# Optimization experiments

Hardware: AMD Instinct MI355X
Metric: run time of the kernel (lower is better)

The kernel has to match this reference:

```python
import jax, jax.numpy as jnp
import numpy as np
from functools import partial

B, T, C, HS = 8, 2048, 2048, 64
H = C // HS
LAYER_ID, N_LAYER, DIVISOR = 12, 24, 8.0


def setup_inputs() -> dict:
    key = jax.random.key(0)
    ks = jax.random.split(key, 6)
    x = jax.random.normal(ks[0], (B, T, C), jnp.float32)
    # faithful RWKV5 parameter initialization
    r01 = LAYER_ID / (N_LAYER - 1)
    r10 = 1.0 - LAYER_ID / N_LAYER
    ddd = np.arange(C, dtype=np.float64) / C
    tmk = (ddd ** r10).reshape(1, 1, C)
    tmv = tmk + 0.3 * r01
    tmr = (ddd ** (0.5 * r10)).reshape(1, 1, C)
    tmg = tmr.copy()
    n = np.arange(C, dtype=np.float64)
    decay = -6.0 + 5.0 * (n / (C - 1)) ** (0.7 + 1.3 * r01)
    zig = ((n + 1) % 3 - 1) * 0.1
    faaaa = r01 * (1.0 - n / (C - 1)) + zig
    f32 = lambda a: jnp.asarray(a, jnp.float32)
    W = lambda k: jax.random.normal(k, (C, C), jnp.float32) * 0.02
    return {
        'x': x,
        'time_mix_k': f32(tmk), 'time_mix_v': f32(tmv),
        'time_mix_r': f32(tmr), 'time_mix_g': f32(tmg),
        'time_decay': f32(decay.reshape(H, HS)),
        'time_faaaa': f32(faaaa.reshape(H, HS)),
        'Wr': W(ks[1]), 'Wk': W(ks[2]), 'Wv': W(ks[3]),
        'Wg': W(ks[4]), 'Wo': W(ks[5]),
        'ln_w': jnp.ones((C,), jnp.float32),
        'ln_b': jnp.zeros((C,), jnp.float32),
    }


def _wkv5(r, k, v, w, u):
    # r,k,v: [B,T,H,N]; w,u: [H,N]; sequential decayed linear attention
    rT = jnp.swapaxes(r, 0, 1)  # [T,B,H,N]
    kT = jnp.swapaxes(k, 0, 1)
    vT = jnp.swapaxes(v, 0, 1)
    wI = w[None, :, :, None]  # decay on key dim i of state S[b,h,i,j]
    uI = u[None, :, :, None]

    def step(S, rkv):
        r_t, k_t, v_t = rkv
        kv = jnp.einsum('bhi,bhj->bhij', k_t, v_t)
        y = jnp.einsum('bhi,bhij->bhj', r_t, S + uI * kv)
        return wI * S + kv, y

    S0 = jnp.zeros((r.shape[0], r.shape[2], r.shape[3], r.shape[3]), r.dtype)
    _, ys = jax.lax.scan(step, S0, (rT, kT, vT))
    return jnp.swapaxes(ys, 0, 1)  # [B,T,H,N]


def reference(x, time_mix_k, time_mix_v, time_mix_r, time_mix_g,
              time_decay, time_faaaa, Wr, Wk, Wv, Wg, Wo, ln_w, ln_b):
    # time shift: prepend zero row, drop last (ZeroPad2d((0,0,1,-1)))
    xx = jnp.pad(x, ((0, 0), (1, 0), (0, 0)))[:, :-1]
    xk = x * time_mix_k + xx * (1.0 - time_mix_k)
    xv = x * time_mix_v + xx * (1.0 - time_mix_v)
    xr = x * time_mix_r + xx * (1.0 - time_mix_r)
    xg = x * time_mix_g + xx * (1.0 - time_mix_g)
    r = (xr @ Wr).reshape(B, T, H, HS)
    k = (xk @ Wk).reshape(B, T, H, HS)
    v = (xv @ Wv).reshape(B, T, H, HS)
    g = jax.nn.silu(xg @ Wg)
    w = jnp.exp(-jnp.exp(time_decay))  # [H,N]
    y = _wkv5(r, k, v, w, time_faaaa)  # [B,T,H,N]
    # GroupNorm(H groups) over head_size, after /head_size_divisor
    yh = y / DIVISOR
    mu = jnp.mean(yh, axis=-1, keepdims=True)
    var = jnp.var(yh, axis=-1, keepdims=True)
    yn = (yh - mu) * jax.lax.rsqrt(var + 1e-5)
    yn = yn * ln_w.reshape(H, HS) + ln_b.reshape(H, HS)
    out = (yn.reshape(B, T, C) * g) @ Wo
    return out
```

## Files before the change

### kernel.cpp

```cpp
#include <hip/hip_runtime.h>
#include <hip/hip_bf16.h>

typedef __bf16 bf16_t;
typedef __bf16 bf16x8 __attribute__((ext_vector_type(8)));
typedef float f32x4 __attribute__((ext_vector_type(4)));

#define Bn 8
#define Tn 2048
#define Cn 2048
#define Hn 32
#define HSn 64
#define CT 64

static const long SZ = (long)Bn * Tn * Cn;

__device__ __forceinline__ void g2l16(const void* g, void* l) {
  __builtin_amdgcn_global_load_lds((const __attribute__((address_space(1))) void*)g,
                                   (__attribute__((address_space(3))) void*)l,
                                   16, 0, 0);
}

template <int CTRL>
__device__ __forceinline__ float dppadd(float x) {
  int yi = __builtin_amdgcn_update_dpp(__float_as_int(x), __float_as_int(x),
                                       CTRL, 0xf, 0xf, false);
  return x + __int_as_float(yi);
}

__global__ __launch_bounds__(256)
void transps(const float* w0, const float* w1, const float* w2,
             const float* w3, const float* w4, bf16_t* oh, bf16_t* ol)
{
  const float* Ws[5] = {w0, w1, w2, w3, w4};
  const float* W = Ws[blockIdx.z];
  const long base = (long)blockIdx.z * ((long)Cn * Cn);
  __shared__ float tile[64][65];
  const int xx = threadIdx.x & 63;
  const int y4 = threadIdx.x >> 6;
  const int bx = blockIdx.x * 64, by = blockIdx.y * 64;
#pragma unroll
  for (int i = 0; i < 16; ++i) {
    int row = i * 4 + y4;
    tile[row][xx] = W[(long)(by + row) * Cn + bx + xx];
  }
  __syncthreads();
#pragma unroll
  for (int i = 0; i < 16; ++i) {
    int row = i * 4 + y4;
    float v = tile[xx][row];
    bf16_t hi = (bf16_t)v;
    long o = base + (long)(bx + row) * Cn + by + xx;
    oh[o] = hi;
    ol[o] = (bf16_t)(v - (float)hi);
  }
}

template <int AMODE, int EMODE>
__global__ __launch_bounds__(512)
void gemmx(const float* __restrict__ X, const float* __restrict__ tm,
           const bf16_t* __restrict__ Ah, const bf16_t* __restrict__ Al,
           const bf16_t* __restrict__ BTh, const bf16_t* __restrict__ BTl,
           void* __restrict__ Cp,
           const bf16_t* __restrict__ Zh, const bf16_t* __restrict__ Zl,
           bf16_t* __restrict__ Gh, bf16_t* __restrict__ Gl)
{
  __shared__ __align__(16) bf16_t lAh[2][256 * 32];
  __shared__ __align__(16) bf16_t lAl[2][256 * 32];
  __shared__ __align__(16) bf16_t lBh[2][256 * 32];
  __shared__ __align__(16) bf16_t lBl[2][256 * 32];

  const int tid = threadIdx.x;
  const int wv = tid >> 6;
  const int lane = tid & 63;
  const int wmw = (wv >> 2) & 1;
  const int wnw = wv & 3;
  const long m0 = (long)blockIdx.y * 256;
  const int n0 = blockIdx.x * 256;

  const int e0 = tid * 8;
  const int e1 = 4096 + tid * 8;
  const int r0 = tid >> 2;
  const int s0 = tid & 3;
  const int c0 = (s0 ^ ((r0 >> 1) & 3)) << 3;
  const long aoff0 = (m0 + r0) * Cn + c0;
  const long aoff1 = (m0 + r0 + 128) * Cn + c0;
  const long boff0 = (long)(n0 + r0) * Cn + c0;
  const long boff1 = (long)(n0 + r0 + 128) * Cn + c0;
  const bool p0ok = ((int)(m0 & (Tn - 1)) | r0) != 0;

  const int kg = lane >> 4;
  const int lr = lane & 15;
  const int kS = (kg ^ ((lr >> 1) & 3)) * 8;

  auto mixA = [&](long kc2, int dst) {
    float xf[16], pf[16], tf[8];
    const long a0 = aoff0 + kc2, a1 = aoff1 + kc2;
    *(f32x4*)&xf[0]  = *(const f32x4*)&X[a0];
    *(f32x4*)&xf[4]  = *(const f32x4*)&X[a0 + 4];
    *(f32x4*)&xf[8]  = *(const f32x4*)&X[a1];
    *(f32x4*)&xf[12] = *(const f32x4*)&X[a1 + 4];
    if (p0ok) {
      *(f32x4*)&pf[0] = *(const f32x4*)&X[a0 - Cn];
      *(f32x4*)&pf[4] = *(const f32x4*)&X[a0 - Cn + 4];
    } else {
#pragma unroll
      for (int q = 0; q < 8; ++q) pf[q] = 0.f;
    }
    *(f32x4*)&pf[8]  = *(const f32x4*)&X[a1 - Cn];
    *(f32x4*)&pf[12] = *(const f32x4*)&X[a1 - Cn + 4];
    *(f32x4*)&tf[0] = *(const f32x4*)&tm[kc2 + c0];
    *(f32x4*)&tf[4] = *(const f32x4*)&tm[kc2 + c0 + 4];
    bf16x8 h0, l0, h1, l1;
#pragma unroll
    for (int q = 0; q < 8; ++q) {
      float o0 = pf[q] + tf[q] * (xf[q] - pf[q]);
      bf16_t hi0 = (bf16_t)o0;
      h0[q] = hi0; l0[q] = (bf16_t)(o0 - (float)hi0);
      float o1 = pf[8 + q] + tf[q] * (xf[8 + q] - pf[8 + q]);
      bf16_t hi1 = (bf16_t)o1;
      h1[q] = hi1; l1[q] = (bf16_t)(o1 - (float)hi1);
    }
    *(bf16x8*)&lAh[dst][e0] = h0; *(bf16x8*)&lAl[dst][e0] = l0;
    *(bf16x8*)&lAh[dst][e1] = h1; *(bf16x8*)&lAl[dst][e1] = l1;
  };

  if constexpr (AMODE == 0) {
    mixA(0, 0);
    g2l16(BTh + boff0, &lBh[0][e0]);
    g2l16(BTh + boff1, &lBh[0][e1]);
    __builtin_amdgcn_sched_barrier(0);
    g2l16(BTl + boff0, &lBl[0][e0]);
    g2l16(BTl + boff1, &lBl[0][e1]);
  } else {
    g2l16(Ah + aoff0, &lAh[0][e0]);
    g2l16(Ah + aoff1, &lAh[0][e1]);
    g2l16(BTh + boff0, &lBh[0][e0]);
    g2l16(BTh + boff1, &lBh[0][e1]);
    __builtin_amdgcn_sched_barrier(0);
    g2l16(Al + aoff0, &lAl[0][e0]);
    g2l16(Al + aoff1, &lAl[0][e1]);
    g2l16(BTl + boff0, &lBl[0][e0]);
    g2l16(BTl + boff1, &lBl[0][e1]);
  }

  const int NT = Cn / 32;
  f32x4 acc[8][4] = {};
  bf16x8 ah[8], bh[4];

  for (int t = 0; t < NT; ++t) {
    const int cb = t & 1, nb = cb ^ 1;
    const int tn = (t + 1 < NT) ? t + 1 : 0;
    const long kc = (long)tn * 32;

    if constexpr (AMODE == 0) {
      asm volatile("s_waitcnt vmcnt(2) lgkmcnt(0)" ::: "memory");
    } else {
      asm volatile("s_waitcnt vmcnt(4)" ::: "memory");
    }
    __builtin_amdgcn_sched_barrier(0);
    __builtin_amdgcn_s_barrier();
    __builtin_amdgcn_sched_barrier(0);
    if constexpr (AMODE == 0) {
      g2l16(BTh + boff0 + kc, &lBh[nb][e0]);
      g2l16(BTh + boff1 + kc, &lBh[nb][e1]);
      g2l16(BTl + boff0 + kc, &lBl[nb][e0]);
      g2l16(BTl + boff1 + kc, &lBl[nb][e1]);
    } else {
      g2l16(Ah + aoff0 + kc, &lAh[nb][e0]);
      g2l16(Ah + aoff1 + kc, &lAh[nb][e1]);
      g2l16(BTh + boff0 + kc, &lBh[nb][e0]);
      g2l16(BTh + boff1 + kc, &lBh[nb][e1]);
    }
#pragma unroll
    for (int i = 0; i < 8; ++i)
      ah[i] = *(const bf16x8*)&lAh[cb][(wmw * 128 + i * 16 + lr) * 32 + kS];
#pragma unroll
    for (int j = 0; j < 4; ++j)
      bh[j] = *(const bf16x8*)&lBh[cb][(wnw * 64 + j * 16 + lr) * 32 + kS];
    __builtin_amdgcn_s_setprio(1);
#pragma unroll
    for (int i = 0; i < 8; ++i)
#pragma unroll
      for (int j = 0; j < 4; ++j)
        acc[i][j] = __builtin_amdgcn_mfma_f32_16x16x32_bf16(ah[i], bh[j], acc[i][j], 0, 0, 0);
    __builtin_amdgcn_s_setprio(0);
    if constexpr (AMODE == 0) mixA(kc, nb);

    asm volatile("s_waitcnt vmcnt(4)" ::: "memory");
    __builtin_amdgcn_sched_barrier(0);
    __builtin_amdgcn_s_barrier();
    __builtin_amdgcn_sched_barrier(0);
    if constexpr (AMODE == 1) {
      g2l16(Al + aoff0 + kc, &lAl[nb][e0]);
      g2l16(Al + aoff1 + kc, &lAl[nb][e1]);
      g2l16(BTl + boff0 + kc, &lBl[nb][e0]);
      g2l16(BTl + boff1 + kc, &lBl[nb][e1]);
    }
    bf16x8 al[8], bl[4];
#pragma unroll
    for (int i = 0; i < 8; ++i)
      al[i] = *(const bf16x8*)&lAl[cb][(wmw * 128 + i * 16 + lr) * 32 + kS];
#pragma unroll
    for (int j = 0; j < 4; ++j)
      bl[j] = *(const bf16x8*)&lBl[cb][(wnw * 64 + j * 16 + lr) * 32 + kS];
    __builtin_amdgcn_s_setprio(1);
#pragma unroll
    for (int i = 0; i < 8; ++i) {
#pragma unroll
      for (int j = 0; j < 4; ++j)
        acc[i][j] = __builtin_amdgcn_mfma_f32_16x16x32_bf16(al[i], bh[j], acc[i][j], 0, 0, 0);
#pragma unroll
      for (int j = 0; j < 4; ++j)
        acc[i][j] = __builtin_amdgcn_mfma_f32_16x16x32_bf16(ah[i], bl[j], acc[i][j], 0, 0, 0);
    }
    __builtin_amdgcn_s_setprio(0);
  }

  const int qr = lane >> 4;
  const int cnn = lane & 15;
#pragma unroll
  for (int i = 0; i < 8; ++i) {
#pragma unroll
    for (int j = 0; j < 4; ++j) {
#pragma unroll
      for (int rg = 0; rg < 4; ++rg) {
        long row = m0 + wmw * 128 + i * 16 + qr * 4 + rg;
        int col = n0 + wnw * 64 + j * 16 + cnn;
        long off = row * Cn + col;
        float vv = acc[i][j][rg];
        if constexpr (EMODE == 0) {
          ((bf16_t*)Cp)[off] = (bf16_t)vv;
        } else if constexpr (EMODE == 1) {
          float z = (float)Zh[off] + (float)Zl[off];
          float zg = vv / (1.f + __expf(-vv)) * z;
          bf16_t hi = (bf16_t)zg;
          Gh[off] = hi;
          Gl[off] = (bf16_t)(zg - (float)hi);
        } else if constexpr (EMODE == 2) {
          ((float*)Cp)[off] = vv;
        } else {
          bf16_t hi = (bf16_t)vv;
          Gh[off] = hi;
          Gl[off] = (bf16_t)(vv - (float)hi);
        }
      }
    }
  }
}

__global__ __launch_bounds__(512)
void wkv5(const bf16_t* Rh, const bf16_t* __restrict__ Rl,
          const bf16_t* Km, const bf16_t* __restrict__ Vm,
          const float* __restrict__ decay, const float* __restrict__ faaaa,
          const float* __restrict__ lw, const float* __restrict__ lb,
          bf16_t* Zh, bf16_t* Zl)
{
  const int bh = blockIdx.x;
  const int b = bh >> 5;
  const int h = bh & 31;
  const int tid = threadIdx.x;
  const int j = tid >> 3;
  const int ic = tid & 7;
  const int i0 = ic * 8;

  float w[8], u[8], S[8];
#pragma unroll
  for (int q = 0; q < 8; ++q) {
    w[q] = expf(-expf(decay[h * 64 + i0 + q]));
    u[q] = faaaa[h * 64 + i0 + q];
    S[q] = 0.f;
  }

  __shared__ __align__(16) float sR[2][CT * 64];
  __shared__ __align__(16) float sK[2][CT * 64];
  __shared__ __align__(16) float sV[2][CT * 64];
  __shared__ __align__(16) float sY[CT * 64];
  __shared__ float sA[2][CT];

  const int e = tid * 8;
  const int tl = e >> 6;
  const int cc = e & 63;
  const long gbase = (long)b * Tn * Cn + h * 64 + cc;

  const int wv = tid >> 6;
  const int ln = tid & 63;
  const float lwv = lw[h * 64 + ln];
  const float lbv = lb[h * 64 + ln];

  bf16x8 prh, prl, pk, pv;
  auto issue = [&](int cch) {
    const long g = gbase + (long)(cch * CT + tl) * Cn;
    prh = *(const bf16x8*)&Rh[g];
    prl = *(const bf16x8*)&Rl[g];
    pk  = *(const bf16x8*)&Km[g];
    pv  = *(const bf16x8*)&Vm[g];
  };
  auto commit = [&](int bufA) {
    float apv = 0.f;
#pragma unroll
    for (int q = 0; q < 8; ++q) {
      float rf = (float)prh[q] + (float)prl[q];
      float kf = (float)pk[q];
      sR[bufA][e + q] = rf;
      sK[bufA][e + q] = kf;
      sV[bufA][e + q] = (float)pv[q];
      apv += (rf * u[q]) * kf;
    }
    apv = dppadd<0xB1>(apv);
    apv = dppadd<0x4E>(apv);
    apv = dppadd<0x141>(apv);
    if (ic == 0) sA[bufA][tl] = apv;
  };

  issue(0); commit(0);
  __syncthreads();
  issue(1);

  const int NC = Tn / CT;
  for (int cch = 0; cch < NC; ++cch) {
    const int buf = cch & 1;
#pragma unroll 4
    for (int t = 0; t < CT; ++t) {
      float rr[8], kk[8];
      *(f32x4*)&rr[0] = *(const f32x4*)&sR[buf][t * 64 + i0];
      *(f32x4*)&rr[4] = *(const f32x4*)&sR[buf][t * 64 + i0 + 4];
      *(f32x4*)&kk[0] = *(const f32x4*)&sK[buf][t * 64 + i0];
      *(f32x4*)&kk[4] = *(const f32x4*)&sK[buf][t * 64 + i0 + 4];
      float vj = sV[buf][t * 64 + j];
      float yp = 0.f;
#pragma unroll
      for (int q = 0; q < 8; ++q) {
        yp += rr[q] * S[q];
        S[q] = w[q] * S[q] + kk[q] * vj;
      }
      yp = dppadd<0xB1>(yp);
      yp = dppadd<0x4E>(yp);
      yp = dppadd<0x141>(yp);
      if (ic == 0) sY[t * 64 + j] = (yp + sA[buf][t] * vj) * 0.125f;
    }
    if (cch + 1 < NC) commit((cch + 1) & 1);
    __syncthreads();
    if (cch + 2 < NC) issue(cch + 2);

    const long zrow0 = ((long)b * Tn + (long)cch * CT) * Cn + h * 64 + ln;
#pragma unroll
    for (int q = 0; q < 8; ++q) {
      const int t = wv * 8 + q;
      float val = sY[t * 64 + ln];
      float s = val, s2 = val * val;
      s = dppadd<0xB1>(s);   s2 = dppadd<0xB1>(s2);
      s = dppadd<0x4E>(s);   s2 = dppadd<0x4E>(s2);
      s = dppadd<0x141>(s);  s2 = dppadd<0x141>(s2);
      s = dppadd<0x140>(s);  s2 = dppadd<0x140>(s2);
      s  += __shfl_xor(s, 16);  s2 += __shfl_xor(s2, 16);
      s  += __shfl_xor(s, 32);  s2 += __shfl_xor(s2, 32);
      float mu = s * (1.f / 64.f);
      float var = fmaxf(s2 * (1.f / 64.f) - mu * mu, 0.f);
      float rs = rsqrtf(var + 1e-5f);
      float zv = (val - mu) * rs * lwv + lbv;
      bf16_t zh = (bf16_t)zv;
      Zh[zrow0 + (long)t * Cn] = zh;
      Zl[zrow0 + (long)t * Cn] = (bf16_t)(zv - (float)zh);
    }
    __syncthreads();
  }
}

extern "C" void kernel_launch(void* const* d_in, const int* in_sizes, int n_in,
                              void* d_out, int out_size, void* d_ws, size_t ws_size,
                              hipStream_t stream)
{
  const float* x    = (const float*)d_in[0];
  const float* tmk  = (const float*)d_in[1];
  const float* tmv  = (const float*)d_in[2];
  const float* tmr  = (const float*)d_in[3];
  const float* tmg  = (const float*)d_in[4];
  const float* tdec = (const float*)d_in[5];
  const float* tfaa = (const float*)d_in[6];
  const float* Wr   = (const float*)d_in[7];
  const float* Wk   = (const float*)d_in[8];
  const float* Wv   = (const float*)d_in[9];
  const float* Wg   = (const float*)d_in[10];
  const float* Wo   = (const float*)d_in[11];
  const float* lnw  = (const float*)d_in[12];
  const float* lnb  = (const float*)d_in[13];

  char* ws = (char*)d_ws;
  const long WSZ = (long)Cn * Cn;
  const long SZB = SZ * 2;
  bf16_t* wTh = (bf16_t*)ws;
  bf16_t* wTl = (bf16_t*)(ws + 5 * WSZ * 2);
  bf16_t* sl0 = (bf16_t*)(ws + 10 * WSZ * 2);
  bf16_t* sl1 = (bf16_t*)(ws + 10 * WSZ * 2 + SZB);
  bf16_t* d0a = (bf16_t*)d_out;
  bf16_t* d0b = (bf16_t*)d_out + SZ;

  const dim3 gGrid(8, 64, 1);

  transps<<<dim3(32, 32, 5), 256, 0, stream>>>(Wr, Wk, Wv, Wg, Wo, wTh, wTl);

  gemmx<0, 3><<<gGrid, 512, 0, stream>>>(x, tmr, nullptr, nullptr,
                                         wTh + 0 * WSZ, wTl + 0 * WSZ, nullptr,
                                         nullptr, nullptr, d0a, sl1);
  gemmx<0, 0><<<gGrid, 512, 0, stream>>>(x, tmk, nullptr, nullptr,
                                         wTh + 1 * WSZ, wTl + 1 * WSZ, d0b,
                                         nullptr, nullptr, nullptr, nullptr);
  gemmx<0, 0><<<gGrid, 512, 0, stream>>>(x, tmv, nullptr, nullptr,
                                         wTh + 2 * WSZ, wTl + 2 * WSZ, sl0,
                                         nullptr, nullptr, nullptr, nullptr);

  wkv5<<<256, 512, 0, stream>>>(d0a, sl1, d0b, sl0, tdec, tfaa, lnw, lnb,
                                d0a, d0b);

  gemmx<0, 1><<<gGrid, 512, 0, stream>>>(x, tmg, nullptr, nullptr,
                                         wTh + 3 * WSZ, wTl + 3 * WSZ, nullptr,
                                         d0a, d0b, sl0, sl1);

  gemmx<1, 2><<<gGrid, 512, 0, stream>>>(nullptr, nullptr, sl0, sl1,
                                         wTh + 4 * WSZ, wTl + 4 * WSZ, d_out,
                                         nullptr, nullptr, nullptr, nullptr);
}
```

Measured before the change: 2.956 ms.

## Split GEMM k-step into barrier-separated phases interleaving LDS reads and MFMA

Restructures the bf16x3-style split GEMM main loop into five phases, each loading a slice of A/B fragments from LDS followed by a barrier and a block of MFMAs. The activation mix/convert is split into halves and interleaved between MFMA phases. This is meant to stagger LDS traffic against matrix work across waves and reduce register pressure, since the low A fragments use 4 registers instead of 8. In exchange it adds many more s_barriers per iteration and a full vmcnt(0) drain at the end of each step, which may serialize the global-to-LDS prefetch.

```diff
diff --git a/kernel.cpp b/kernel.cpp
--- a/kernel.cpp
+++ b/kernel.cpp
@@ -91,44 +91,39 @@
   const int kg = lane >> 4;
   const int lr = lane & 15;
   const int kS = (kg ^ ((lr >> 1) & 3)) * 8;
-
-  auto mixA = [&](long kc2, int dst) {
-    float xf[16], pf[16], tf[8];
-    const long a0 = aoff0 + kc2, a1 = aoff1 + kc2;
-    *(f32x4*)&xf[0]  = *(const f32x4*)&X[a0];
-    *(f32x4*)&xf[4]  = *(const f32x4*)&X[a0 + 4];
-    *(f32x4*)&xf[8]  = *(const f32x4*)&X[a1];
-    *(f32x4*)&xf[12] = *(const f32x4*)&X[a1 + 4];
-    if (p0ok) {
-      *(f32x4*)&pf[0] = *(const f32x4*)&X[a0 - Cn];
-      *(f32x4*)&pf[4] = *(const f32x4*)&X[a0 - Cn + 4];
+  const int aBase = (wmw * 128 + lr) * 32 + kS;
+  const int bBase = (wnw * 64 + lr) * 32 + kS;
+
+  auto mixHalf = [&](long kc2, int dst, int half) {
+    const long a = (half ? aoff1 : aoff0) + kc2;
+    const int edst = half ? e1 : e0;
+    float xf[8], pf[8], tf[8];
+    *(f32x4*)&xf[0] = *(const f32x4*)&X[a];
+    *(f32x4*)&xf[4] = *(const f32x4*)&X[a + 4];
+    if (half || p0ok) {
+      *(f32x4*)&pf[0] = *(const f32x4*)&X[a - Cn];
+      *(f32x4*)&pf[4] = *(const f32x4*)&X[a - Cn + 4];
     } else {
 #pragma unroll
       for (int q = 0; q < 8; ++q) pf[q] = 0.f;
     }
-    *(f32x4*)&pf[8]  = *(const f32x4*)&X[a1 - Cn];
-    *(f32x4*)&pf[12] = *(const f32x4*)&X[a1 - Cn + 4];
     *(f32x4*)&tf[0] = *(const f32x4*)&tm[kc2 + c0];
     *(f32x4*)&tf[4] = *(const f32x4*)&tm[kc2 + c0 + 4];
-    bf16x8 h0, l0, h1, l1;
+    bf16x8 hh, ll;
 #pragma unroll
     for (int q = 0; q < 8; ++q) {
-      float o0 = pf[q] + tf[q] * (xf[q] - pf[q]);
-      bf16_t hi0 = (bf16_t)o0;
-      h0[q] = hi0; l0[q] = (bf16_t)(o0 - (float)hi0);
-      float o1 = pf[8 + q] + tf[q] * (xf[8 + q] - pf[8 + q]);
-      bf16_t hi1 = (bf16_t)o1;
-      h1[q] = hi1; l1[q] = (bf16_t)(o1 - (float)hi1);
-    }
-    *(bf16x8*)&lAh[dst][e0] = h0; *(bf16x8*)&lAl[dst][e0] = l0;
-    *(bf16x8*)&lAh[dst][e1] = h1; *(bf16x8*)&lAl[dst][e1] = l1;
+      float o = pf[q] + tf[q] * (xf[q] - pf[q]);
+      bf16_t hi = (bf16_t)o;
+      hh[q] = hi; ll[q] = (bf16_t)(o - (float)hi);
+    }
+    *(bf16x8*)&lAh[dst][edst] = hh;
+    *(bf16x8*)&lAl[dst][edst] = ll;
   };
 
   if constexpr (AMODE == 0) {
-    mixA(0, 0);
+    mixHalf(0, 0, 0); mixHalf(0, 0, 1);
     g2l16(BTh + boff0, &lBh[0][e0]);
     g2l16(BTh + boff1, &lBh[0][e1]);
-    __builtin_amdgcn_sched_barrier(0);
     g2l16(BTl + boff0, &lBl[0][e0]);
     g2l16(BTl + boff1, &lBl[0][e1]);
   } else {
@@ -136,84 +131,122 @@
     g2l16(Ah + aoff1, &lAh[0][e1]);
     g2l16(BTh + boff0, &lBh[0][e0]);
     g2l16(BTh + boff1, &lBh[0][e1]);
-    __builtin_amdgcn_sched_barrier(0);
     g2l16(Al + aoff0, &lAl[0][e0]);
     g2l16(Al + aoff1, &lAl[0][e1]);
     g2l16(BTl + boff0, &lBl[0][e0]);
     g2l16(BTl + boff1, &lBl[0][e1]);
   }
+  asm volatile("s_waitcnt vmcnt(0) lgkmcnt(0)" ::: "memory");
+  __syncthreads();
 
   const int NT = Cn / 32;
   f32x4 acc[8][4] = {};
-  bf16x8 ah[8], bh[4];
+  bf16x8 ah[8], bh[4], al[4], bl[4];
 
   for (int t = 0; t < NT; ++t) {
     const int cb = t & 1, nb = cb ^ 1;
     const int tn = (t + 1 < NT) ? t + 1 : 0;
     const long kc = (long)tn * 32;
 
-    if constexpr (AMODE == 0) {
-      asm volatile("s_waitcnt vmcnt(2) lgkmcnt(0)" ::: "memory");
-    } else {
-      asm volatile("s_waitcnt vmcnt(4)" ::: "memory");
-    }
-    __builtin_amdgcn_sched_barrier(0);
-    __builtin_amdgcn_s_barrier();
-    __builtin_amdgcn_sched_barrier(0);
+#pragma unroll
+    for (int i = 0; i < 4; ++i)
+      ah[i] = *(const bf16x8*)&lAh[cb][aBase + i * 512];
+#pragma unroll
+    for (int j = 0; j < 4; ++j)
+      bh[j] = *(const bf16x8*)&lBh[cb][bBase + j * 512];
     if constexpr (AMODE == 0) {
       g2l16(BTh + boff0 + kc, &lBh[nb][e0]);
       g2l16(BTh + boff1 + kc, &lBh[nb][e1]);
-      g2l16(BTl + boff0 + kc, &lBl[nb][e0]);
-      g2l16(BTl + boff1 + kc, &lBl[nb][e1]);
     } else {
       g2l16(Ah + aoff0 + kc, &lAh[nb][e0]);
       g2l16(Ah + aoff1 + kc, &lAh[nb][e1]);
       g2l16(BTh + boff0 + kc, &lBh[nb][e0]);
       g2l16(BTh + boff1 + kc, &lBh[nb][e1]);
     }
-#pragma unroll
-    for (int i = 0; i < 8; ++i)
-      ah[i] = *(const bf16x8*)&lAh[cb][(wmw * 128 + i * 16 + lr) * 32 + kS];
-#pragma unroll
-    for (int j = 0; j < 4; ++j)
-      bh[j] = *(const bf16x8*)&lBh[cb][(wnw * 64 + j * 16 + lr) * 32 + kS];
+    __builtin_amdgcn_s_barrier();
+    asm volatile("s_waitcnt lgkmcnt(0)" ::: "memory");
+    __builtin_amdgcn_sched_barrier(0);
     __builtin_amdgcn_s_setprio(1);
 #pragma unroll
-    for (int i = 0; i < 8; ++i)
+    for (int i = 0; i < 4; ++i)
 #pragma unroll
       for (int j = 0; j < 4; ++j)
         acc[i][j] = __builtin_amdgcn_mfma_f32_16x16x32_bf16(ah[i], bh[j], acc[i][j], 0, 0, 0);
     __builtin_amdgcn_s_setprio(0);
-    if constexpr (AMODE == 0) mixA(kc, nb);
-
-    asm volatile("s_waitcnt vmcnt(4)" ::: "memory");
-    __builtin_amdgcn_sched_barrier(0);
-    __builtin_amdgcn_s_barrier();
-    __builtin_amdgcn_sched_barrier(0);
-    if constexpr (AMODE == 1) {
+    __builtin_amdgcn_s_barrier();
+
+#pragma unroll
+    for (int i = 0; i < 4; ++i)
+      ah[4 + i] = *(const bf16x8*)&lAh[cb][aBase + (4 + i) * 512];
+    if constexpr (AMODE == 0) {
+      g2l16(BTl + boff0 + kc, &lBl[nb][e0]);
+      g2l16(BTl + boff1 + kc, &lBl[nb][e1]);
+    } else {
       g2l16(Al + aoff0 + kc, &lAl[nb][e0]);
       g2l16(Al + aoff1 + kc, &lAl[nb][e1]);
       g2l16(BTl + boff0 + kc, &lBl[nb][e0]);
       g2l16(BTl + boff1 + kc, &lBl[nb][e1]);
     }
-    bf16x8 al[8], bl[4];
-#pragma unroll
-    for (int i = 0; i < 8; ++i)
-      al[i] = *(const bf16x8*)&lAl[cb][(wmw * 128 + i * 16 + lr) * 32 + kS];
-#pragma unroll
-    for (int j = 0; j < 4; ++j)
-      bl[j] = *(const bf16x8*)&lBl[cb][(wnw * 64 + j * 16 + lr) * 32 + kS];
+    __builtin_amdgcn_s_barrier();
+    asm volatile("s_waitcnt lgkmcnt(0)" ::: "memory");
+    __builtin_amdgcn_sched_barrier(0);
     __builtin_amdgcn_s_setprio(1);
 #pragma unroll
-    for (int i = 0; i < 8; ++i) {
+    for (int i = 0; i < 4; ++i)
+#pragma unroll
+      for (int j = 0; j < 4; ++j)
+        acc[4 + i][j] = __builtin_amdgcn_mfma_f32_16x16x32_bf16(ah[4 + i], bh[j], acc[4 + i][j], 0, 0, 0);
+    __builtin_amdgcn_s_setprio(0);
+    __builtin_amdgcn_s_barrier();
+
+#pragma unroll
+    for (int i = 0; i < 4; ++i)
+      al[i] = *(const bf16x8*)&lAl[cb][aBase + i * 512];
+    __builtin_amdgcn_s_barrier();
+    asm volatile("s_waitcnt lgkmcnt(0)" ::: "memory");
+    __builtin_amdgcn_sched_barrier(0);
+    __builtin_amdgcn_s_setprio(1);
+#pragma unroll
+    for (int i = 0; i < 4; ++i)
 #pragma unroll
       for (int j = 0; j < 4; ++j)
         acc[i][j] = __builtin_amdgcn_mfma_f32_16x16x32_bf16(al[i], bh[j], acc[i][j], 0, 0, 0);
+    __builtin_amdgcn_s_setprio(0);
+    if constexpr (AMODE == 0) mixHalf(kc, nb, 0);
+    __builtin_amdgcn_s_barrier();
+
+#pragma unroll
+    for (int i = 0; i < 4; ++i)
+      al[i] = *(const bf16x8*)&lAl[cb][aBase + (4 + i) * 512];
+    __builtin_amdgcn_s_barrier();
+    asm volatile("s_waitcnt lgkmcnt(0)" ::: "memory");
+    __builtin_amdgcn_sched_barrier(0);
+    __builtin_amdgcn_s_setprio(1);
+#pragma unroll
+    for (int i = 0; i < 4; ++i)
+#pragma unroll
+      for (int j = 0; j < 4; ++j)
+        acc[4 + i][j] = __builtin_amdgcn_mfma_f32_16x16x32_bf16(al[i], bh[j], acc[4 + i][j], 0, 0, 0);
+    __builtin_amdgcn_s_setprio(0);
+    if constexpr (AMODE == 0) mixHalf(kc, nb, 1);
+    __builtin_amdgcn_s_barrier();
+
+#pragma unroll
+    for (int j = 0; j < 4; ++j)
+      bl[j] = *(const bf16x8*)&lBl[cb][bBase + j * 512];
+    __builtin_amdgcn_s_barrier();
+    asm volatile("s_waitcnt lgkmcnt(0)" ::: "memory");
+    __builtin_amdgcn_sched_barrier(0);
+    __builtin_amdgcn_s_setprio(1);
+#pragma unroll
+    for (int i = 0; i < 8; ++i)
 #pragma unroll
       for (int j = 0; j < 4; ++j)
         acc[i][j] = __builtin_amdgcn_mfma_f32_16x16x32_bf16(ah[i], bl[j], acc[i][j], 0, 0, 0);
-    }
     __builtin_amdgcn_s_setprio(0);
+    asm volatile("s_waitcnt vmcnt(0)" ::: "memory");
+    __builtin_amdgcn_sched_barrier(0);
+    __builtin_amdgcn_s_barrier();
   }
 
   const int qr = lane >> 4;
```

Result: slower. 3.290 ms (+11.3%).
